# Kernel optimization log

Measured on AMD Instinct MI355X. Metric: run time of the kernel, lower is better.

The kernel has to match this reference:

```python
import jax, jax.numpy as jnp
import numpy as np

N = 50000
E = 800000
D_IN = 64
D_OUT = 64


def setup_inputs() -> dict:
    key = jax.random.key(0)
    k_x, k_e, k_ws, k_bs, k_wn, k_bn = jax.random.split(key, 6)
    x = jax.random.normal(k_x, (N, D_IN), dtype=jnp.float32)
    edge_index = jax.random.randint(k_e, (2, E), 0, N, dtype=jnp.int64)
    # nn.Linear params: weight [out, in], bias [out]
    lim = 1.0 / np.sqrt(D_IN)
    W_self = jax.random.uniform(k_ws, (D_OUT, D_IN), minval=-lim, maxval=lim, dtype=jnp.float32)
    b_self = jax.random.uniform(k_bs, (D_OUT,), minval=-lim, maxval=lim, dtype=jnp.float32)
    W_neigh = jax.random.uniform(k_wn, (D_OUT, D_IN), minval=-lim, maxval=lim, dtype=jnp.float32)
    b_neigh = jax.random.uniform(k_bn, (D_OUT,), minval=-lim, maxval=lim, dtype=jnp.float32)
    return {"x": x, "edge_index": edge_index, "W_self": W_self, "b_self": b_self,
            "W_neigh": W_neigh, "b_neigh": b_neigh}


def reference(x, edge_index, W_self, b_self, W_neigh, b_neigh):
    row, col = edge_index[0], edge_index[1]
    n = x.shape[0]
    # degree of each destination node (clamped to 1)
    deg = jax.ops.segment_sum(jnp.ones_like(row, dtype=x.dtype), row, num_segments=n)
    deg = jnp.maximum(deg, 1.0)
    # mean-aggregate neighbor features: scatter-add x[col] into row buckets
    agg = jax.ops.segment_sum(x[col], row, num_segments=n)  # [N, D_IN]
    agg = agg / deg[:, None]
    out = x @ W_self.T + b_self + agg @ W_neigh.T + b_neigh
    return out
```

## Files before the change

### kernel.cpp

```cpp
#include <hip/hip_runtime.h>
#include <hip/hip_bf16.h>


#define D    64
#define CAP  64
#define TPB  256
#define WPB  4
#define TPW  16
#define EPT  8
#define CAPB 4608

typedef __attribute__((ext_vector_type(8))) short bf16x8;
typedef __attribute__((ext_vector_type(4))) float f32x4;

__device__ __forceinline__ unsigned short f2bf(float f) {
    unsigned u = __float_as_uint(f);
    return (unsigned short)((u + 0x7fffu + ((u >> 16) & 1u)) >> 16);
}
__device__ __forceinline__ float bf2f(unsigned short s) {
    return __uint_as_float((unsigned)s << 16);
}

__device__ __forceinline__ int load_idx(const void* ei, int use64, long long pos) {
    if (use64) return (int)((const long long*)ei)[pos];
    return ((const int*)ei)[pos];
}

__global__ __launch_bounds__(256) void init_k(
        const long long* __restrict__ ei, const float* __restrict__ x,
        unsigned short* __restrict__ xb, unsigned* __restrict__ gcur,
        int* __restrict__ flag, int N, int NBr) {
    int tid = blockIdx.x * 256 + threadIdx.x;
    int NT  = gridDim.x * 256;
    for (int i = tid; i < NBr; i += NT) gcur[i] = 0u;
    int NV = (N * D) >> 2;
    for (int i = tid; i < NV; i += NT) {
        float4 v = *(const float4*)&x[i * 4];
        ushort4 o;
        o.x = f2bf(v.x); o.y = f2bf(v.y); o.z = f2bf(v.z); o.w = f2bf(v.w);
        *(ushort4*)&xb[i * 4] = o;
    }
    if (blockIdx.x == 0 && threadIdx.x < 64) {
        int t = threadIdx.x;
        long long v = (t < 16) ? ei[t] : 0;
        unsigned long long bad = __ballot(t < 16 && (v < 0 || v >= (long long)N));
        if (t == 0) *flag = (bad == 0ULL) ? 1 : 0;
    }
}

__global__ __launch_bounds__(256) void bin_k(
        const void* __restrict__ ei, const int* __restrict__ flag,
        unsigned* __restrict__ staging, unsigned* __restrict__ gcur,
        int N, int E, int NBr) {
    __shared__ unsigned lcnt[256];
    __shared__ unsigned lbase[256];
    const int t = threadIdx.x;
    lcnt[t] = 0u;
    __syncthreads();
    const int use64 = *flag;
    const int e0 = blockIdx.x * (256 * EPT);
    unsigned pk[EPT], lp[EPT];
    int bk[EPT];
    #pragma unroll
    for (int j = 0; j < EPT; ++j) {
        int e = e0 + j * 256 + t;
        if (e < E) {
            int r = load_idx(ei, use64, e);
            int c = load_idx(ei, use64, (long long)E + e);
            pk[j] = ((unsigned)r << 16) | (unsigned)(c & 0xffff);
            bk[j] = r >> 8;
            lp[j] = atomicAdd(&lcnt[bk[j]], 1u);
        } else bk[j] = -1;
    }
    __syncthreads();
    if (t < NBr) {
        unsigned n = lcnt[t];
        lbase[t] = n ? atomicAdd(&gcur[t], n) : 0u;
    }
    __syncthreads();
    #pragma unroll
    for (int j = 0; j < EPT; ++j) {
        if (bk[j] >= 0) {
            unsigned p = lbase[bk[j]] + lp[j];
            if (p < CAPB) staging[(unsigned)bk[j] * CAPB + p] = pk[j];
        }
    }
}

__global__ __launch_bounds__(256) void bucket_k(
        const unsigned* __restrict__ staging, const unsigned* __restrict__ gcur,
        int* __restrict__ cnt, unsigned short* __restrict__ slots, int N) {
    __shared__ unsigned short sl[256 * CAP];
    __shared__ unsigned scnt[256];
    const int t = threadIdx.x, b = blockIdx.x;
    scnt[t] = 0u;
    __syncthreads();
    unsigned nb = gcur[b]; if (nb > CAPB) nb = CAPB;
    for (unsigned e = t; e < nb; e += 256) {
        unsigned pk = staging[(unsigned)b * CAPB + e];
        unsigned rl = (pk >> 16) & 255u;
        unsigned pos = atomicAdd(&scnt[rl], 1u);
        if (pos < CAP) sl[(rl << 6) + pos] = (unsigned short)(pk & 0xffffu);
    }
    __syncthreads();
    int n0 = b << 8;
    int nn = N - n0; if (nn > 256) nn = 256;
    const uint4* s4 = (const uint4*)sl;
    uint4* g4 = (uint4*)&slots[(size_t)n0 * CAP];
    for (int i = t; i < nn * 8; i += 256) g4[i] = s4[i];
    if (t < nn) cnt[n0 + t] = (int)scnt[t];
}

__global__ __launch_bounds__(TPB) void fused_k(
        const unsigned short* __restrict__ xb,
        const int* __restrict__ cnt, const unsigned short* __restrict__ slots,
        const float* __restrict__ Ws, const float* __restrict__ bs,
        const float* __restrict__ Wn, const float* __restrict__ bn,
        float* __restrict__ out, int N) {
    __shared__ __align__(16) short wcat[D][136];
    __shared__ __align__(16) short mtile[WPB][TPW][72];

    const int t = threadIdx.x;
    for (int i = t; i < D * 128; i += TPB) {
        int f = i >> 7, kk = i & 127;
        float v = (kk < D) ? Ws[f * D + kk] : Wn[f * D + (kk - D)];
        wcat[f][kk] = (short)f2bf(v);
    }
    __syncthreads();

    const int w    = t >> 6;
    const int lane = t & 63;
    const int m_   = lane & 15;
    const int quad = lane >> 4;
    const int ql   = m_;
    const int q4   = quad;

    int tile = (blockIdx.x * WPB + w) * TPW;
    if (tile >= N) return;

    for (int p = 0; p < 4; ++p) {
        int n = tile + p * 4 + q4;
        int deg = (n < N) ? cnt[n] : 0;
        int mm = deg < CAP ? deg : CAP;
        float4 s = make_float4(0.f, 0.f, 0.f, 0.f);
        for (int base = 0; base < mm; base += 16) {
            int sv = (base + ql < mm) ? (int)slots[n * CAP + base + ql] : 0;
            int mq = mm - base; if (mq > 16) mq = 16;
            unsigned off[16];
            #pragma unroll
            for (int j = 0; j < 16; ++j) {
                int c = __shfl(sv, (q4 << 4) + j);
                off[j] = (unsigned)c * D + 4 * ql;
            }
            ushort4 v[16];
            #pragma unroll
            for (int j = 0; j < 16; ++j)
                v[j] = *(const ushort4*)&xb[off[j]];
            #pragma unroll
            for (int j = 0; j < 16; ++j) {
                float m = (j < mq) ? 1.0f : 0.0f;
                s.x = fmaf(m, bf2f(v[j].x), s.x);
                s.y = fmaf(m, bf2f(v[j].y), s.y);
                s.z = fmaf(m, bf2f(v[j].z), s.z);
                s.w = fmaf(m, bf2f(v[j].w), s.w);
            }
        }
        float dinv = (deg > 0) ? 1.0f / (float)deg : 0.0f;
        short4 mv;
        mv.x = (short)f2bf(s.x * dinv); mv.y = (short)f2bf(s.y * dinv);
        mv.z = (short)f2bf(s.z * dinv); mv.w = (short)f2bf(s.w * dinv);
        *(short4*)&mtile[w][p * 4 + q4][4 * ql] = mv;
    }

    int nrow = tile + m_;
    const unsigned short* xr = xb + (size_t)(nrow < N ? nrow : 0) * D;
    bf16x8 afrag[4];
    afrag[0] = *(const bf16x8*)&xr[quad * 8];
    afrag[1] = *(const bf16x8*)&xr[32 + quad * 8];
    #pragma unroll
    for (int ks = 2; ks < 4; ++ks)
        afrag[ks] = *(const bf16x8*)&mtile[w][m_][(ks - 2) * 32 + quad * 8];

    f32x4 acc[4];
    #pragma unroll
    for (int nf = 0; nf < 4; ++nf) {
        int fcol = nf * 16 + m_;
        float bsum = bs[fcol] + bn[fcol];
        acc[nf] = (f32x4){bsum, bsum, bsum, bsum};
    }
    #pragma unroll
    for (int nf = 0; nf < 4; ++nf) {
        #pragma unroll
        for (int ks = 0; ks < 4; ++ks) {
            bf16x8 bfr = *(const bf16x8*)&wcat[nf * 16 + m_][ks * 32 + quad * 8];
            acc[nf] = __builtin_amdgcn_mfma_f32_16x16x32_bf16(
                afrag[ks], bfr, acc[nf], 0, 0, 0);
        }
    }

    #pragma unroll
    for (int nf = 0; nf < 4; ++nf) {
        int fcol = nf * 16 + m_;
        #pragma unroll
        for (int r = 0; r < 4; ++r) {
            int node = tile + quad * 4 + r;
            if (node < N) out[(size_t)node * D + fcol] = acc[nf][r];
        }
    }
}

extern "C" void kernel_launch(void* const* d_in, const int* in_sizes, int n_in,
                              void* d_out, int out_size, void* d_ws, size_t ws_size,
                              hipStream_t stream) {
    const float* x  = (const float*)d_in[0];
    const void*  ei = d_in[1];
    const float* Ws = (const float*)d_in[2];
    const float* bs = (const float*)d_in[3];
    const float* Wn = (const float*)d_in[4];
    const float* bn = (const float*)d_in[5];
    float* out = (float*)d_out;

    int N = in_sizes[0] / D;
    int E = in_sizes[1] / 2;

    unsigned short* xb    = (unsigned short*)d_ws;
    unsigned short* slots = xb + (size_t)N * D;
    int*            cnt   = (int*)(slots + (size_t)N * CAP);
    int*            flag  = cnt + N;

    int NBr = (N + 255) >> 8;
    unsigned* staging = (unsigned*)d_out;
    unsigned* gcur    = staging + (size_t)NBr * CAPB;

    init_k<<<1024, 256, 0, stream>>>((const long long*)ei, x, xb, gcur, flag, N, NBr);

    int binb = (E + 256 * EPT - 1) / (256 * EPT);
    bin_k<<<binb, 256, 0, stream>>>(ei, flag, staging, gcur, N, E, NBr);

    bucket_k<<<NBr, 256, 0, stream>>>(staging, gcur, cnt, slots, N);

    int ntiles  = (N + TPW - 1) / TPW;
    int fblocks = (ntiles + WPB - 1) / WPB;
    fused_k<<<fblocks, TPB, 0, stream>>>(xb, cnt, slots, Ws, bs, Wn, bn, out, N);
}
```

Baseline: 125.1 us.

## Fold init into bin kernel and split each tile across two waves

Removes the separate init kernel. The bf16 conversion of x and the index-width check move into the binning kernel, and the bucket-counter reset becomes a memset. In the fused kernel, each 16-node tile is now shared by two waves: each wave aggregates half of the rows and computes half of the output columns, synchronised with a block barrier. This doubles the number of blocks and cuts per-wave serial gather work, aiming at more parallelism and one fewer launch. The cost is an added __syncthreads, and every block now reloads the weight tile, for twice as many blocks.

```diff
diff --git a/kernel.cpp b/kernel.cpp
--- a/kernel.cpp
+++ b/kernel.cpp
@@ -5,8 +5,9 @@
 #define D    64
 #define CAP  64
 #define TPB  256
-#define WPB  4
 #define TPW  16
+#define WPT  2
+#define TPBL 2
 #define EPT  8
 #define CAPB 4608
 
@@ -26,38 +27,22 @@
     return ((const int*)ei)[pos];
 }
 
-__global__ __launch_bounds__(256) void init_k(
-        const long long* __restrict__ ei, const float* __restrict__ x,
-        unsigned short* __restrict__ xb, unsigned* __restrict__ gcur,
-        int* __restrict__ flag, int N, int NBr) {
-    int tid = blockIdx.x * 256 + threadIdx.x;
-    int NT  = gridDim.x * 256;
-    for (int i = tid; i < NBr; i += NT) gcur[i] = 0u;
-    int NV = (N * D) >> 2;
-    for (int i = tid; i < NV; i += NT) {
-        float4 v = *(const float4*)&x[i * 4];
-        ushort4 o;
-        o.x = f2bf(v.x); o.y = f2bf(v.y); o.z = f2bf(v.z); o.w = f2bf(v.w);
-        *(ushort4*)&xb[i * 4] = o;
-    }
-    if (blockIdx.x == 0 && threadIdx.x < 64) {
-        int t = threadIdx.x;
-        long long v = (t < 16) ? ei[t] : 0;
-        unsigned long long bad = __ballot(t < 16 && (v < 0 || v >= (long long)N));
-        if (t == 0) *flag = (bad == 0ULL) ? 1 : 0;
-    }
-}
-
 __global__ __launch_bounds__(256) void bin_k(
-        const void* __restrict__ ei, const int* __restrict__ flag,
+        const float* __restrict__ x, const void* __restrict__ ei,
         unsigned* __restrict__ staging, unsigned* __restrict__ gcur,
-        int N, int E, int NBr) {
+        unsigned short* __restrict__ xb, int N, int E, int NBr) {
     __shared__ unsigned lcnt[256];
     __shared__ unsigned lbase[256];
+    __shared__ int s_use64;
     const int t = threadIdx.x;
     lcnt[t] = 0u;
-    __syncthreads();
-    const int use64 = *flag;
+    if (t < 64) {
+        long long v = (t < 16) ? ((const long long*)ei)[t] : 0;
+        unsigned long long bad = __ballot(t < 16 && (v < 0 || v >= (long long)N));
+        if (t == 0) s_use64 = (bad == 0ULL) ? 1 : 0;
+    }
+    __syncthreads();
+    const int use64 = s_use64;
     const int e0 = blockIdx.x * (256 * EPT);
     unsigned pk[EPT], lp[EPT];
     int bk[EPT];
@@ -85,6 +70,15 @@
             if (p < CAPB) staging[(unsigned)bk[j] * CAPB + p] = pk[j];
         }
     }
+    int tid = blockIdx.x * 256 + t;
+    int NT  = gridDim.x * 256;
+    int NV  = (N * D) >> 2;
+    for (int i = tid; i < NV; i += NT) {
+        float4 v = *(const float4*)&x[i * 4];
+        ushort4 o;
+        o.x = f2bf(v.x); o.y = f2bf(v.y); o.z = f2bf(v.z); o.w = f2bf(v.w);
+        *(ushort4*)&xb[i * 4] = o;
+    }
 }
 
 __global__ __launch_bounds__(256) void bucket_k(
@@ -118,7 +112,7 @@
         const float* __restrict__ Wn, const float* __restrict__ bn,
         float* __restrict__ out, int N) {
     __shared__ __align__(16) short wcat[D][136];
-    __shared__ __align__(16) short mtile[WPB][TPW][72];
+    __shared__ __align__(16) short mtile[TPBL][TPW][72];
 
     const int t = threadIdx.x;
     for (int i = t; i < D * 128; i += TPB) {
@@ -134,11 +128,14 @@
     const int quad = lane >> 4;
     const int ql   = m_;
     const int q4   = quad;
-
-    int tile = (blockIdx.x * WPB + w) * TPW;
-    if (tile >= N) return;
-
-    for (int p = 0; p < 4; ++p) {
+    const int pair = w >> 1;
+    const int half = w & 1;
+
+    const int tile = (blockIdx.x * TPBL + pair) * TPW;
+
+    #pragma unroll
+    for (int pp = 0; pp < 2; ++pp) {
+        int p = half * 2 + pp;
         int n = tile + p * 4 + q4;
         int deg = (n < N) ? cnt[n] : 0;
         int mm = deg < CAP ? deg : CAP;
@@ -169,8 +166,9 @@
         short4 mv;
         mv.x = (short)f2bf(s.x * dinv); mv.y = (short)f2bf(s.y * dinv);
         mv.z = (short)f2bf(s.z * dinv); mv.w = (short)f2bf(s.w * dinv);
-        *(short4*)&mtile[w][p * 4 + q4][4 * ql] = mv;
-    }
+        *(short4*)&mtile[pair][p * 4 + q4][4 * ql] = mv;
+    }
+    __syncthreads();
 
     int nrow = tile + m_;
     const unsigned short* xr = xb + (size_t)(nrow < N ? nrow : 0) * D;
@@ -179,32 +177,33 @@
     afrag[1] = *(const bf16x8*)&xr[32 + quad * 8];
     #pragma unroll
     for (int ks = 2; ks < 4; ++ks)
-        afrag[ks] = *(const bf16x8*)&mtile[w][m_][(ks - 2) * 32 + quad * 8];
-
-    f32x4 acc[4];
-    #pragma unroll
-    for (int nf = 0; nf < 4; ++nf) {
-        int fcol = nf * 16 + m_;
+        afrag[ks] = *(const bf16x8*)&mtile[pair][m_][(ks - 2) * 32 + quad * 8];
+
+    f32x4 acc[2];
+    #pragma unroll
+    for (int i = 0; i < 2; ++i) {
+        int fcol = (half * 2 + i) * 16 + m_;
         float bsum = bs[fcol] + bn[fcol];
-        acc[nf] = (f32x4){bsum, bsum, bsum, bsum};
-    }
-    #pragma unroll
-    for (int nf = 0; nf < 4; ++nf) {
+        acc[i] = (f32x4){bsum, bsum, bsum, bsum};
+    }
+    #pragma unroll
+    for (int i = 0; i < 2; ++i) {
+        int nf = half * 2 + i;
         #pragma unroll
         for (int ks = 0; ks < 4; ++ks) {
             bf16x8 bfr = *(const bf16x8*)&wcat[nf * 16 + m_][ks * 32 + quad * 8];
-            acc[nf] = __builtin_amdgcn_mfma_f32_16x16x32_bf16(
-                afrag[ks], bfr, acc[nf], 0, 0, 0);
-        }
-    }
-
-    #pragma unroll
-    for (int nf = 0; nf < 4; ++nf) {
-        int fcol = nf * 16 + m_;
+            acc[i] = __builtin_amdgcn_mfma_f32_16x16x32_bf16(
+                afrag[ks], bfr, acc[i], 0, 0, 0);
+        }
+    }
+
+    #pragma unroll
+    for (int i = 0; i < 2; ++i) {
+        int fcol = (half * 2 + i) * 16 + m_;
         #pragma unroll
         for (int r = 0; r < 4; ++r) {
             int node = tile + quad * 4 + r;
-            if (node < N) out[(size_t)node * D + fcol] = acc[nf][r];
+            if (node < N) out[(size_t)node * D + fcol] = acc[i][r];
         }
     }
 }
@@ -226,20 +225,19 @@
     unsigned short* xb    = (unsigned short*)d_ws;
     unsigned short* slots = xb + (size_t)N * D;
     int*            cnt   = (int*)(slots + (size_t)N * CAP);
-    int*            flag  = cnt + N;
 
     int NBr = (N + 255) >> 8;
     unsigned* staging = (unsigned*)d_out;
     unsigned* gcur    = staging + (size_t)NBr * CAPB;
 
-    init_k<<<1024, 256, 0, stream>>>((const long long*)ei, x, xb, gcur, flag, N, NBr);
+    hipMemsetAsync(gcur, 0, (size_t)NBr * sizeof(unsigned), stream);
 
     int binb = (E + 256 * EPT - 1) / (256 * EPT);
-    bin_k<<<binb, 256, 0, stream>>>(ei, flag, staging, gcur, N, E, NBr);
+    bin_k<<<binb, 256, 0, stream>>>(x, ei, staging, gcur, xb, N, E, NBr);
 
     bucket_k<<<NBr, 256, 0, stream>>>(staging, gcur, cnt, slots, N);
 
     int ntiles  = (N + TPW - 1) / TPW;
-    int fblocks = (ntiles + WPB - 1) / WPB;
+    int fblocks = (ntiles + TPBL - 1) / TPBL;
     fused_k<<<fblocks, TPB, 0, stream>>>(xb, cnt, slots, Ws, bs, Wn, bn, out, N);
 }
```

After: 126.1 us. Within noise of the previous version (+0.8%).
